# Kernel tuning notes

Measured on AMD Instinct MI355X. Metric: run time of the kernel, lower is better.

The kernel has to match this reference:

```python
import jax, jax.numpy as jnp
import numpy as np

SEQ, B, IN, H = 512, 64, 256, 512

def _lin_params(key, out_d, in_d):
    k1, k2 = jax.random.split(key)
    bound = 1.0 / np.sqrt(in_d)
    w = jax.random.uniform(k1, (out_d, in_d), jnp.float32, -bound, bound)
    b = jax.random.uniform(k2, (out_d,), jnp.float32, -bound, bound)
    return w, b

def setup_inputs() -> dict:
    key = jax.random.key(0)
    ks = jax.random.split(key, 9)
    x = jax.random.normal(ks[0], (SEQ, B, IN), jnp.float32)
    h0 = jnp.zeros((B, H), jnp.float32)
    c0 = jnp.zeros((B, H), jnp.float32)
    Wf_w, Wf_b = _lin_params(ks[1], H, IN)
    Uf_w, Uf_b = _lin_params(ks[2], H, H)
    Wi_w, Wi_b = _lin_params(ks[3], H, IN)
    Ui_w, Ui_b = _lin_params(ks[4], H, H)
    Wo_w, Wo_b = _lin_params(ks[5], H, IN)
    Uo_w, Uo_b = _lin_params(ks[6], H, H)
    Wc_w, Wc_b = _lin_params(ks[7], H, IN)
    Uc_w, Uc_b = _lin_params(ks[8], H, H)
    return dict(x=x, h0=h0, c0=c0,
                Wf_w=Wf_w, Wf_b=Wf_b, Uf_w=Uf_w, Uf_b=Uf_b,
                Wi_w=Wi_w, Wi_b=Wi_b, Ui_w=Ui_w, Ui_b=Ui_b,
                Wo_w=Wo_w, Wo_b=Wo_b, Uo_w=Uo_w, Uo_b=Uo_b,
                Wc_w=Wc_w, Wc_b=Wc_b, Uc_w=Uc_w, Uc_b=Uc_b)

def reference(x, h0, c0,
              Wf_w, Wf_b, Uf_w, Uf_b,
              Wi_w, Wi_b, Ui_w, Ui_b,
              Wo_w, Wo_b, Uo_w, Uo_b,
              Wc_w, Wc_b, Uc_w, Uc_b):
    # Precompute all input-to-hidden projections in one batched GEMM per gate.
    xf = jnp.einsum('tbi,hi->tbh', x, Wf_w) + Wf_b  # (T,B,H)
    xi = jnp.einsum('tbi,hi->tbh', x, Wi_w) + Wi_b
    xo = jnp.einsum('tbi,hi->tbh', x, Wo_w) + Wo_b
    xc = jnp.einsum('tbi,hi->tbh', x, Wc_w) + Wc_b

    def step(carry, xs):
        h, c = carry
        xft, xit, xot, xct = xs
        f = jax.nn.sigmoid(xft + h @ Uf_w.T + Uf_b)
        i = jax.nn.sigmoid(xit + h @ Ui_w.T + Ui_b)
        o = jax.nn.sigmoid(xot + h @ Uo_w.T + Uo_b)
        c = f * c + i * jnp.tanh(xct + h @ Uc_w.T + Uc_b)
        h = o * jnp.tanh(c)
        return (h, c), h

    (h, c), h_seq = jax.lax.scan(step, (h0, c0), (xf, xi, xo, xc))
    return h_seq, h, c
```

## Files before the change

kernel.cpp:

```cpp
#include <hip/hip_runtime.h>


#define T_STEPS 512
#define BATCH   64
#define IN_D    256
#define HID     512
#define NGROUP  4
#define NSLICE  16
#define BLK_B   16
#define BLK_H   32
#define THREADS 512

using short8  = __attribute__((ext_vector_type(8))) short;
using float4v = __attribute__((ext_vector_type(4))) float;

#define FRAG_ADDR(f) (((f) << 4) + (((f) >> 4) << 4))

__device__ __forceinline__ unsigned short f2bf(float f) {
    union { float f; unsigned int i; } v; v.f = f;
    unsigned int r = v.i + 0x7fff + ((v.i >> 16) & 1);
    return (unsigned short)(r >> 16);
}
__device__ __forceinline__ short8 pack8(float4 a, float4 b) {
    short8 s;
    s[0]=(short)f2bf(a.x); s[1]=(short)f2bf(a.y); s[2]=(short)f2bf(a.z); s[3]=(short)f2bf(a.w);
    s[4]=(short)f2bf(b.x); s[5]=(short)f2bf(b.y); s[6]=(short)f2bf(b.z); s[7]=(short)f2bf(b.w);
    return s;
}
__device__ __forceinline__ float sigm(float v) { return 1.0f / (1.0f + __expf(-v)); }
__device__ __forceinline__ float tanh_(float v) { return 2.0f / (1.0f + __expf(-2.0f * v)) - 1.0f; }

__global__ __launch_bounds__(256, 1) void lstm_init_flags(unsigned int* flags, int n) {
    int i = blockIdx.x * blockDim.x + threadIdx.x;
    if (i < n) flags[i] = 0u;
}

__global__ __launch_bounds__(THREADS, 2) void lstm_persist(
    const float* __restrict__ x,
    const float* __restrict__ h0,
    const float* __restrict__ c0,
    const float* __restrict__ Wf, const float* __restrict__ Wfb,
    const float* __restrict__ Uf, const float* __restrict__ Ufb,
    const float* __restrict__ Wi, const float* __restrict__ Wib,
    const float* __restrict__ Ui, const float* __restrict__ Uib,
    const float* __restrict__ Wo, const float* __restrict__ Wob,
    const float* __restrict__ Uo, const float* __restrict__ Uob,
    const float* __restrict__ Wc, const float* __restrict__ Wcb,
    const float* __restrict__ Uc, const float* __restrict__ Ucb,
    float* out,
    unsigned int* flags)
{
    __shared__ __attribute__((aligned(16))) unsigned char hfrag[17392];
    __shared__ __attribute__((aligned(16))) unsigned char xfrag[8688];
    __shared__ float g_lds[8 * 256];

    const int tid  = threadIdx.x;
    const int lane = tid & 63;
    const int wave = tid >> 6;
    const int gate = wave >> 1;
    const int hlf  = wave & 1;
    const int grp  = blockIdx.x & 3;
    const int slc  = blockIdx.x >> 2;
    const int bb   = grp * BLK_B;
    const int hbase= slc * BLK_H;
    const int lm   = lane & 15;
    const int lq   = lane >> 4;
    const int row  = tid >> 5;
    const int seg  = tid & 31;

    const float* Ug  = (gate == 0) ? Uf : (gate == 1) ? Ui : (gate == 2) ? Uo : Uc;
    const float* Wg  = (gate == 0) ? Wf : (gate == 1) ? Wi : (gate == 2) ? Wo : Wc;
    const float* Wbg = (gate == 0) ? Wfb : (gate == 1) ? Wib : (gate == 2) ? Wob : Wcb;
    const float* Ubg = (gate == 0) ? Ufb : (gate == 1) ? Uib : (gate == 2) ? Uob : Ucb;
    const int ng = hbase + hlf * 16 + lm;

    short8 ufrag[16];
#pragma unroll
    for (int ks = 0; ks < 16; ++ks) {
        const float* p = Ug + (size_t)ng * HID + ks * 32 + lq * 8;
        ufrag[ks] = pack8(*(const float4*)(p), *(const float4*)(p + 4));
    }
    short8 wfrag[8];
#pragma unroll
    for (int ks = 0; ks < 8; ++ks) {
        const float* p = Wg + (size_t)ng * IN_D + ks * 32 + lq * 8;
        wfrag[ks] = pack8(*(const float4*)(p), *(const float4*)(p + 4));
    }
    const float bias = Wbg[ng] + Ubg[ng];

    float c_reg = c0[(size_t)(bb + row) * HID + hbase + seg];

    {
        const float* ph = h0 + (size_t)(bb + row) * HID + seg * 16;
        int f0 = (seg >> 1) * 64 + (seg & 1) * 32 + row;
        *(short8*)(hfrag + FRAG_ADDR(f0))      = pack8(*(const float4*)(ph),     *(const float4*)(ph + 4));
        *(short8*)(hfrag + FRAG_ADDR(f0 + 16)) = pack8(*(const float4*)(ph + 8), *(const float4*)(ph + 12));

        const float* px = x + (size_t)(bb + row) * IN_D + seg * 8;
        int fx = (seg >> 2) * 64 + (seg & 3) * 16 + row;
        *(short8*)(xfrag + FRAG_ADDR(fx)) = pack8(*(const float4*)(px), *(const float4*)(px + 4));
    }
    float4 xn0, xn1;
    {
        const float* px = x + ((size_t)1 * BATCH + bb + row) * IN_D + seg * 8;
        xn0 = *(const float4*)(px); xn1 = *(const float4*)(px + 4);
    }
    __syncthreads();

    float4v accx0 = {bias, bias, bias, bias};
    float4v accx1 = {0.f, 0.f, 0.f, 0.f};
#pragma unroll
    for (int ks = 0; ks < 8; ++ks) {
        short8 a = *(const short8*)(xfrag + FRAG_ADDR(ks * 64 + lane));
        if (ks & 1) accx1 = __builtin_amdgcn_mfma_f32_16x16x32_bf16(a, wfrag[ks], accx1, 0, 0, 0);
        else        accx0 = __builtin_amdgcn_mfma_f32_16x16x32_bf16(a, wfrag[ks], accx0, 0, 0, 0);
    }

    unsigned int* const cnt = flags + (size_t)grp * T_STEPS;
    float* const out_h = out + (size_t)T_STEPS * BATCH * HID;
    float* const out_c = out_h + (size_t)BATCH * HID;

    for (int t = 0; t < T_STEPS; ++t) {
        float4v acc0 = accx0, acc1 = accx1;
#pragma unroll
        for (int ks = 0; ks < 16; ++ks) {
            short8 a = *(const short8*)(hfrag + FRAG_ADDR(ks * 64 + lane));
            if (ks & 1) acc1 = __builtin_amdgcn_mfma_f32_16x16x32_bf16(a, ufrag[ks], acc1, 0, 0, 0);
            else        acc0 = __builtin_amdgcn_mfma_f32_16x16x32_bf16(a, ufrag[ks], acc0, 0, 0, 0);
        }
        float4v acc = acc0 + acc1;
#pragma unroll
        for (int r = 0; r < 4; ++r)
            g_lds[wave * 256 + (lq * 4 + r) * 16 + lm] = acc[r];
        __syncthreads();

        float hv;
        {
            int hf2 = seg >> 4, nn = seg & 15;
            float fpre = g_lds[(0 * 2 + hf2) * 256 + row * 16 + nn];
            float ipre = g_lds[(1 * 2 + hf2) * 256 + row * 16 + nn];
            float opre = g_lds[(2 * 2 + hf2) * 256 + row * 16 + nn];
            float gpre = g_lds[(3 * 2 + hf2) * 256 + row * 16 + nn];
            float fv = sigm(fpre), iv = sigm(ipre), ov = sigm(opre);
            float gv = tanh_(gpre);
            c_reg = fv * c_reg + iv * gv;
            hv = ov * tanh_(c_reg);
        }
        __hip_atomic_store(out + ((size_t)t * BATCH + bb + row) * HID + hbase + seg,
                           hv, __ATOMIC_RELAXED, __HIP_MEMORY_SCOPE_AGENT);
        if (t == T_STEPS - 1) {
            out_h[(size_t)(bb + row) * HID + hbase + seg] = hv;
            out_c[(size_t)(bb + row) * HID + hbase + seg] = c_reg;
        }

        if (t + 1 < T_STEPS) {
            int fx = (seg >> 2) * 64 + (seg & 3) * 16 + row;
            *(short8*)(xfrag + FRAG_ADDR(fx)) = pack8(xn0, xn1);
            int tn = (t + 2 < T_STEPS) ? (t + 2) : (T_STEPS - 1);
            const float* px = x + ((size_t)tn * BATCH + bb + row) * IN_D + seg * 8;
            xn0 = *(const float4*)(px); xn1 = *(const float4*)(px + 4);
        }

        asm volatile("s_waitcnt vmcnt(0)" ::: "memory");
        __syncthreads();

        if (t + 1 < T_STEPS) {
            if (tid == 0)
                __hip_atomic_fetch_add(&cnt[t], 1u, __ATOMIC_RELAXED, __HIP_MEMORY_SCOPE_AGENT);

            accx0 = (float4v){bias, bias, bias, bias};
            accx1 = (float4v){0.f, 0.f, 0.f, 0.f};
#pragma unroll
            for (int ks = 0; ks < 8; ++ks) {
                short8 a = *(const short8*)(xfrag + FRAG_ADDR(ks * 64 + lane));
                if (ks & 1) accx1 = __builtin_amdgcn_mfma_f32_16x16x32_bf16(a, wfrag[ks], accx1, 0, 0, 0);
                else        accx0 = __builtin_amdgcn_mfma_f32_16x16x32_bf16(a, wfrag[ks], accx0, 0, 0, 0);
            }

            if (tid == 0) {
                while (__hip_atomic_load(&cnt[t], __ATOMIC_RELAXED, __HIP_MEMORY_SCOPE_AGENT)
                       < (unsigned)NSLICE) {  }
            }
            __syncthreads();

            {
                const float* src = out + ((size_t)t * BATCH + bb + row) * HID + seg * 16;
                float4 a0 = *(const float4*)(src);
                float4 a1 = *(const float4*)(src + 4);
                float4 a2 = *(const float4*)(src + 8);
                float4 a3 = *(const float4*)(src + 12);
                int f0 = (seg >> 1) * 64 + (seg & 1) * 32 + row;
                *(short8*)(hfrag + FRAG_ADDR(f0))      = pack8(a0, a1);
                *(short8*)(hfrag + FRAG_ADDR(f0 + 16)) = pack8(a2, a3);
            }
            __syncthreads();
        }
    }
}

extern "C" void kernel_launch(void* const* d_in, const int* in_sizes, int n_in,
                              void* d_out, int out_size, void* d_ws, size_t ws_size,
                              hipStream_t stream) {
    (void)in_sizes; (void)n_in; (void)out_size; (void)ws_size;
    const float* x   = (const float*)d_in[0];
    const float* h0  = (const float*)d_in[1];
    const float* c0  = (const float*)d_in[2];
    const float* Wf  = (const float*)d_in[3];
    const float* Wfb = (const float*)d_in[4];
    const float* Uf  = (const float*)d_in[5];
    const float* Ufb = (const float*)d_in[6];
    const float* Wi  = (const float*)d_in[7];
    const float* Wib = (const float*)d_in[8];
    const float* Ui  = (const float*)d_in[9];
    const float* Uib = (const float*)d_in[10];
    const float* Wo  = (const float*)d_in[11];
    const float* Wob = (const float*)d_in[12];
    const float* Uo  = (const float*)d_in[13];
    const float* Uob = (const float*)d_in[14];
    const float* Wc  = (const float*)d_in[15];
    const float* Wcb = (const float*)d_in[16];
    const float* Uc  = (const float*)d_in[17];
    const float* Ucb = (const float*)d_in[18];

    unsigned int* flags = (unsigned int*)d_ws;
    const int nflags = NGROUP * T_STEPS;

    lstm_init_flags<<<(nflags + 255) / 256, 256, 0, stream>>>(flags, nflags);
    lstm_persist<<<NGROUP * NSLICE, THREADS, 0, stream>>>(
        x, h0, c0,
        Wf, Wfb, Uf, Ufb, Wi, Wib, Ui, Uib,
        Wo, Wob, Uo, Uob, Wc, Wcb, Uc, Ucb,
        (float*)d_out, flags);
}
```

Measured before the change: 1.565 ms.

## Exchange hidden state via bf16 ring buffer with per-slice flags

Each block now writes its bf16-packed hidden slice, already in MFMA fragment layout, into a 4-deep global ring buffer. Consumers can then copy it straight into LDS instead of reloading fp32 h from the output and converting it. The shared atomic counter is replaced by per-slice monotonic flags, which a full wave polls with a ballot. The change also pads the gate LDS buffer to avoid bank conflicts, splits the recurrent MFMA chain into four accumulators, and moves the x prefetch after the vmcnt wait. The aim is to cut inter-block synchronization latency and global traffic on the serial critical path. It relies on relaxed-ordering visibility across blocks and on a ring depth of 4 being enough to prevent overwrites.

```diff
diff --git a/kernel.cpp b/kernel.cpp
--- a/kernel.cpp
+++ b/kernel.cpp
@@ -10,6 +10,9 @@
 #define BLK_B   16
 #define BLK_H   32
 #define THREADS 512
+#define RING    4
+#define RING_BYTES 16384
+#define GSTRIDE 288
 
 using short8  = __attribute__((ext_vector_type(8))) short;
 using float4v = __attribute__((ext_vector_type(4))) float;
@@ -30,9 +33,8 @@
 __device__ __forceinline__ float sigm(float v) { return 1.0f / (1.0f + __expf(-v)); }
 __device__ __forceinline__ float tanh_(float v) { return 2.0f / (1.0f + __expf(-2.0f * v)) - 1.0f; }
 
-__global__ __launch_bounds__(256, 1) void lstm_init_flags(unsigned int* flags, int n) {
-    int i = blockIdx.x * blockDim.x + threadIdx.x;
-    if (i < n) flags[i] = 0u;
+__global__ __launch_bounds__(64, 1) void lstm_init_flags(unsigned int* flags) {
+    flags[threadIdx.x] = 0u;
 }
 
 __global__ __launch_bounds__(THREADS, 2) void lstm_persist(
@@ -48,11 +50,11 @@
     const float* __restrict__ Wc, const float* __restrict__ Wcb,
     const float* __restrict__ Uc, const float* __restrict__ Ucb,
     float* out,
-    unsigned int* flags)
+    unsigned char* ws)
 {
-    __shared__ __attribute__((aligned(16))) unsigned char hfrag[17392];
-    __shared__ __attribute__((aligned(16))) unsigned char xfrag[8688];
-    __shared__ float g_lds[8 * 256];
+    __shared__ __attribute__((aligned(16))) unsigned char hfrag[17408];
+    __shared__ __attribute__((aligned(16))) unsigned char xfrag[8704];
+    __shared__ float g_lds[8 * GSTRIDE];
 
     const int tid  = threadIdx.x;
     const int lane = tid & 63;
@@ -116,38 +118,54 @@
         else        accx0 = __builtin_amdgcn_mfma_f32_16x16x32_bf16(a, wfrag[ks], accx0, 0, 0, 0);
     }
 
-    unsigned int* const cnt = flags + (size_t)grp * T_STEPS;
+    unsigned int* const flagg = (unsigned int*)ws + grp * NSLICE;
+    unsigned char* const ring = ws + 16384 + grp * (RING * RING_BYTES);
     float* const out_h = out + (size_t)T_STEPS * BATCH * HID;
     float* const out_c = out_h + (size_t)BATCH * HID;
 
     for (int t = 0; t < T_STEPS; ++t) {
-        float4v acc0 = accx0, acc1 = accx1;
+        float4v a0 = accx0, a1 = accx1;
+        float4v a2 = {0.f, 0.f, 0.f, 0.f}, a3 = {0.f, 0.f, 0.f, 0.f};
 #pragma unroll
         for (int ks = 0; ks < 16; ++ks) {
             short8 a = *(const short8*)(hfrag + FRAG_ADDR(ks * 64 + lane));
-            if (ks & 1) acc1 = __builtin_amdgcn_mfma_f32_16x16x32_bf16(a, ufrag[ks], acc1, 0, 0, 0);
-            else        acc0 = __builtin_amdgcn_mfma_f32_16x16x32_bf16(a, ufrag[ks], acc0, 0, 0, 0);
-        }
-        float4v acc = acc0 + acc1;
+            switch (ks & 3) {
+                case 0: a0 = __builtin_amdgcn_mfma_f32_16x16x32_bf16(a, ufrag[ks], a0, 0, 0, 0); break;
+                case 1: a1 = __builtin_amdgcn_mfma_f32_16x16x32_bf16(a, ufrag[ks], a1, 0, 0, 0); break;
+                case 2: a2 = __builtin_amdgcn_mfma_f32_16x16x32_bf16(a, ufrag[ks], a2, 0, 0, 0); break;
+                default:a3 = __builtin_amdgcn_mfma_f32_16x16x32_bf16(a, ufrag[ks], a3, 0, 0, 0); break;
+            }
+        }
+        float4v acc = (a0 + a2) + (a1 + a3);
 #pragma unroll
         for (int r = 0; r < 4; ++r)
-            g_lds[wave * 256 + (lq * 4 + r) * 16 + lm] = acc[r];
+            g_lds[wave * GSTRIDE + (lq * 4 + r) * 18 + lm] = acc[r];
         __syncthreads();
 
+        unsigned char* const slot = ring + (size_t)(t & (RING - 1)) * RING_BYTES;
         float hv;
         {
             int hf2 = seg >> 4, nn = seg & 15;
-            float fpre = g_lds[(0 * 2 + hf2) * 256 + row * 16 + nn];
-            float ipre = g_lds[(1 * 2 + hf2) * 256 + row * 16 + nn];
-            float opre = g_lds[(2 * 2 + hf2) * 256 + row * 16 + nn];
-            float gpre = g_lds[(3 * 2 + hf2) * 256 + row * 16 + nn];
+            float fpre = g_lds[(0 * 2 + hf2) * GSTRIDE + row * 18 + nn];
+            float ipre = g_lds[(1 * 2 + hf2) * GSTRIDE + row * 18 + nn];
+            float opre = g_lds[(2 * 2 + hf2) * GSTRIDE + row * 18 + nn];
+            float gpre = g_lds[(3 * 2 + hf2) * GSTRIDE + row * 18 + nn];
             float fv = sigm(fpre), iv = sigm(ipre), ov = sigm(opre);
             float gv = tanh_(gpre);
             c_reg = fv * c_reg + iv * gv;
             hv = ov * tanh_(c_reg);
         }
-        __hip_atomic_store(out + ((size_t)t * BATCH + bb + row) * HID + hbase + seg,
-                           hv, __ATOMIC_RELAXED, __HIP_MEMORY_SCOPE_AGENT);
+        {
+            unsigned short h16 = f2bf(hv);
+            unsigned int partner = ((unsigned int)__shfl_xor((int)h16, 1)) & 0xffffu;
+            if ((seg & 1) == 0) {
+                unsigned int word = ((unsigned int)h16) | (partner << 16);
+                unsigned int* dst = (unsigned int*)(slot + slc * 1024 + (seg >> 3) * 256
+                                                    + row * 16 + (seg & 7) * 2);
+                __hip_atomic_store(dst, word, __ATOMIC_RELAXED, __HIP_MEMORY_SCOPE_AGENT);
+            }
+        }
+        out[((size_t)t * BATCH + bb + row) * HID + hbase + seg] = hv;
         if (t == T_STEPS - 1) {
             out_h[(size_t)(bb + row) * HID + hbase + seg] = hv;
             out_c[(size_t)(bb + row) * HID + hbase + seg] = c_reg;
@@ -156,17 +174,21 @@
         if (t + 1 < T_STEPS) {
             int fx = (seg >> 2) * 64 + (seg & 3) * 16 + row;
             *(short8*)(xfrag + FRAG_ADDR(fx)) = pack8(xn0, xn1);
+        }
+
+        asm volatile("s_waitcnt vmcnt(0)" ::: "memory");
+
+        if (t + 1 < T_STEPS) {
             int tn = (t + 2 < T_STEPS) ? (t + 2) : (T_STEPS - 1);
             const float* px = x + ((size_t)tn * BATCH + bb + row) * IN_D + seg * 8;
             xn0 = *(const float4*)(px); xn1 = *(const float4*)(px + 4);
         }
-
-        asm volatile("s_waitcnt vmcnt(0)" ::: "memory");
         __syncthreads();
 
         if (t + 1 < T_STEPS) {
             if (tid == 0)
-                __hip_atomic_fetch_add(&cnt[t], 1u, __ATOMIC_RELAXED, __HIP_MEMORY_SCOPE_AGENT);
+                __hip_atomic_store(&flagg[slc], (unsigned)(t + 1),
+                                   __ATOMIC_RELAXED, __HIP_MEMORY_SCOPE_AGENT);
 
             accx0 = (float4v){bias, bias, bias, bias};
             accx1 = (float4v){0.f, 0.f, 0.f, 0.f};
@@ -177,21 +199,29 @@
                 else        accx0 = __builtin_amdgcn_mfma_f32_16x16x32_bf16(a, wfrag[ks], accx0, 0, 0, 0);
             }
 
-            if (tid == 0) {
-                while (__hip_atomic_load(&cnt[t], __ATOMIC_RELAXED, __HIP_MEMORY_SCOPE_AGENT)
-                       < (unsigned)NSLICE) {  }
+            if (wave == 0) {
+                bool need = lane < NSLICE;
+                while (true) {
+                    unsigned v = need ? __hip_atomic_load(&flagg[lane], __ATOMIC_RELAXED,
+                                                          __HIP_MEMORY_SCOPE_AGENT)
+                                      : 0xffffffffu;
+                    if (__ballot(need && (v < (unsigned)(t + 1))) == 0ull) break;
+                }
             }
             __syncthreads();
 
             {
-                const float* src = out + ((size_t)t * BATCH + bb + row) * HID + seg * 16;
-                float4 a0 = *(const float4*)(src);
-                float4 a1 = *(const float4*)(src + 4);
-                float4 a2 = *(const float4*)(src + 8);
-                float4 a3 = *(const float4*)(src + 12);
-                int f0 = (seg >> 1) * 64 + (seg & 1) * 32 + row;
-                *(short8*)(hfrag + FRAG_ADDR(f0))      = pack8(a0, a1);
-                *(short8*)(hfrag + FRAG_ADDR(f0 + 16)) = pack8(a2, a3);
+                const unsigned long long* src =
+                    (const unsigned long long*)(slot) + (size_t)tid * 4;
+                unsigned long long d0 = __hip_atomic_load(src + 0, __ATOMIC_RELAXED, __HIP_MEMORY_SCOPE_AGENT);
+                unsigned long long d1 = __hip_atomic_load(src + 1, __ATOMIC_RELAXED, __HIP_MEMORY_SCOPE_AGENT);
+                unsigned long long d2 = __hip_atomic_load(src + 2, __ATOMIC_RELAXED, __HIP_MEMORY_SCOPE_AGENT);
+                unsigned long long d3 = __hip_atomic_load(src + 3, __ATOMIC_RELAXED, __HIP_MEMORY_SCOPE_AGENT);
+                unsigned char* dst = hfrag + 32 * tid + 16 * (tid >> 3);
+                *(unsigned long long*)(dst)      = d0;
+                *(unsigned long long*)(dst + 8)  = d1;
+                *(unsigned long long*)(dst + 16) = d2;
+                *(unsigned long long*)(dst + 24) = d3;
             }
             __syncthreads();
         }
@@ -222,13 +252,10 @@
     const float* Uc  = (const float*)d_in[17];
     const float* Ucb = (const float*)d_in[18];
 
-    unsigned int* flags = (unsigned int*)d_ws;
-    const int nflags = NGROUP * T_STEPS;
-
-    lstm_init_flags<<<(nflags + 255) / 256, 256, 0, stream>>>(flags, nflags);
+    lstm_init_flags<<<1, 64, 0, stream>>>((unsigned int*)d_ws);
     lstm_persist<<<NGROUP * NSLICE, THREADS, 0, stream>>>(
         x, h0, c0,
         Wf, Wfb, Uf, Ufb, Wi, Wib, Ui, Uib,
         Wo, Wob, Uo, Uob, Wc, Wcb, Uc, Ucb,
-        (float*)d_out, flags);
-}
+        (float*)d_out, (unsigned char*)d_ws);
+}
```

After: 1.627 ms. +3.9%, slower.
